# Kernel optimization log

Measured on AMD Instinct MI355X. Metric: run time of the kernel, lower is better.

Reference implementation:

```python
import jax, jax.numpy as jnp
import numpy as np

LEAK_VALUE = 0.1
B, N_ATOMS, IN_F, H, MAX_VAL, OUT_F = 256, 128, 128, 256, 6, 256


def gru(x, W_ih, W_hh, b_ih, b_hh):
    # x: [B, T, in]; W_ih: [3H, in]; W_hh: [3H, H]; gate order r,z,n (torch)
    Bb, T, _ = x.shape
    Hh = W_hh.shape[1]
    x_proj = jnp.einsum('bti,gi->btg', x, W_ih) + b_ih  # [B, T, 3H]

    def step(h, xp):
        gh = h @ W_hh.T + b_hh                      # [B, 3H]
        xr, xz, xn = jnp.split(xp, 3, axis=-1)
        hr, hz, hn = jnp.split(gh, 3, axis=-1)
        r = jax.nn.sigmoid(xr + hr)
        z = jax.nn.sigmoid(xz + hz)
        n = jnp.tanh(xn + r * hn)
        h_new = (1.0 - z) * n + z * h
        return h_new, h_new

    h0 = jnp.zeros((Bb, Hh), x.dtype)
    _, out = jax.lax.scan(step, h0, jnp.swapaxes(x_proj, 0, 1))  # [T, B, H]
    return jnp.swapaxes(out, 0, 1)  # [B, T, H]


def setup_inputs() -> dict:
    key = jax.random.key(0)
    ks = jax.random.split(key, 8)
    s = 0.05
    return {
        'x': jax.random.normal(ks[0], (B, N_ATOMS, IN_F), jnp.float32),
        'bonded_atoms': jax.random.randint(ks[1], (B, N_ATOMS, MAX_VAL), 0, N_ATOMS),
        'W_ih': jax.random.normal(ks[2], (3 * H, IN_F), jnp.float32) * s,
        'W_hh': jax.random.normal(ks[3], (3 * H, H), jnp.float32) * s,
        'b_ih': jax.random.normal(ks[4], (3 * H,), jnp.float32) * s,
        'b_hh': jax.random.normal(ks[5], (3 * H,), jnp.float32) * s,
        'W_fc': jax.random.normal(ks[6], (OUT_F, H * MAX_VAL), jnp.float32) * s,
        'b_fc': jax.random.normal(ks[7], (OUT_F,), jnp.float32) * s,
    }


def reference(x, bonded_atoms, W_ih, W_hh, b_ih, b_hh, W_fc, b_fc):
    rnn_out = gru(x, W_ih, W_hh, b_ih, b_hh)               # [B, N, H]
    batch_idx = jnp.arange(x.shape[0])[:, None, None]       # [B, 1, 1]
    fc_in = rnn_out[batch_idx, bonded_atoms]                # [B, N, V, H] gather
    fc_in = fc_in.reshape(x.shape[0], x.shape[1], -1)       # [B, N, V*H]
    out = fc_in @ W_fc.T + b_fc                             # [B, N, OUT_F]
    return jnp.where(out >= 0, out, LEAK_VALUE * out)
```

## Files before the change

### kernel.cpp

```cpp
#include <hip/hip_runtime.h>
#include <hip/hip_bf16.h>
#include <stdint.h>

typedef unsigned short u16;
typedef __bf16 bf16_t;
typedef bf16_t bf16x8 __attribute__((ext_vector_type(8)));
typedef u16    u16x8  __attribute__((ext_vector_type(8)));
typedef u16    u16x4  __attribute__((ext_vector_type(4)));
typedef float  f32x4  __attribute__((ext_vector_type(4)));

#define BSZ    256
#define NATOMS 128
#define INF    128
#define HH     256
#define H3     768
#define MAXV   6
#define OUTF   256
#define KFC    (HH * MAXV)
#define PLANE  8388608
#define HAP    264

__device__ __forceinline__ u16 f2bf(float f) {
  union { float f; unsigned u; } v; v.f = f;
  unsigned u = v.u;
  unsigned r = (u + 0x7FFFu + ((u >> 16) & 1u)) >> 16;
  return (u16)r;
}
__device__ __forceinline__ float bf2f(u16 h) {
  union { unsigned u; float f; } v; v.u = ((unsigned)h) << 16;
  return v.f;
}
__device__ __forceinline__ f32x4 mfma_bf16(u16x8 a, u16x8 b, f32x4 c) {
  return __builtin_amdgcn_mfma_f32_16x16x32_bf16(
      __builtin_bit_cast(bf16x8, a), __builtin_bit_cast(bf16x8, b), c, 0, 0, 0);
}
__device__ __forceinline__ float sel4(float a0, float a1, float a2, float a3, int q) {
  float t01 = (q & 1) ? a1 : a0;
  float t23 = (q & 1) ? a3 : a2;
  return (q & 2) ? t23 : t01;
}

#define NX4   1048576
#define C1    1048576
#define C2    1073152
#define C3    1122304
#define C4    1220608
__global__ void k_prep4(const float* __restrict__ x, const float* __restrict__ wih,
                        const float* __restrict__ whh, const float* __restrict__ wfc,
                        u16* __restrict__ xb, u16* __restrict__ wihb,
                        u16* __restrict__ whhb, u16* __restrict__ wfcb) {
  int i = blockIdx.x * 256 + threadIdx.x;
  const float* src; u16* dst; int j;
  if (i < C1)      { src = x;   dst = xb;   j = i; }
  else if (i < C2) { src = wih; dst = wihb; j = i - C1; }
  else if (i < C3) { src = whh; dst = whhb; j = i - C2; }
  else             { src = wfc; dst = wfcb; j = i - C3; }
  f32x4 v = *(const f32x4*)(src + (size_t)j * 4);
  u16x4 o;
#pragma unroll
  for (int k = 0; k < 4; k++) o[k] = f2bf(v[k]);
  *(u16x4*)(dst + (size_t)j * 4) = o;
}

__global__ __launch_bounds__(256) void k_xproj(const u16* __restrict__ X,
                                               const u16* __restrict__ W,
                                               const float* __restrict__ bias,
                                               const float* __restrict__ bhh,
                                               u16* __restrict__ out) {
  __shared__ __align__(16) u16 As[128][136];
  __shared__ __align__(16) u16 Bs[128][136];
  const int tid = threadIdx.x, lane = tid & 63, wid = tid >> 6;
  const int c16 = lane & 15, quad = lane >> 4;
  const int wm = (wid & 1) * 64, wn = (wid >> 1) * 64;
  const int bg = blockIdx.x >> 2, tg = blockIdx.x & 3;
  const int n0 = blockIdx.y * 128;

#pragma unroll
  for (int j = 0; j < 8; j++) {
    const int u = tid + j * 256, row = u >> 4, ch = u & 15;
    const int b = bg * 4 + (row & 3), t = tg * 32 + (row >> 2);
    *(u16x8*)&As[row][ch * 8] =
        *(const u16x8*)(X + ((size_t)b * 16384 + t * 128 + ch * 8));
    *(u16x8*)&Bs[row][ch * 8] =
        *(const u16x8*)(W + ((size_t)(n0 + row) * 128 + ch * 8));
  }
  __syncthreads();

  const f32x4 zero = {0.f, 0.f, 0.f, 0.f};
  f32x4 acc[4][4];
#pragma unroll
  for (int mi = 0; mi < 4; mi++)
#pragma unroll
    for (int ni = 0; ni < 4; ni++) acc[mi][ni] = zero;

#pragma unroll
  for (int kt = 0; kt < 4; kt++) {
    u16x8 af[4], bf[4];
#pragma unroll
    for (int mi = 0; mi < 4; mi++)
      af[mi] = *(const u16x8*)&As[wm + mi * 16 + c16][kt * 32 + quad * 8];
#pragma unroll
    for (int ni = 0; ni < 4; ni++)
      bf[ni] = *(const u16x8*)&Bs[wn + ni * 16 + c16][kt * 32 + quad * 8];
#pragma unroll
    for (int mi = 0; mi < 4; mi++)
#pragma unroll
      for (int ni = 0; ni < 4; ni++)
        acc[mi][ni] = mfma_bf16(af[mi], bf[ni], acc[mi][ni]);
  }

  const int bb = bg >> 2, mbh = bg & 3;
#pragma unroll
  for (int ni = 0; ni < 4; ni++) {
    const int n = n0 + wn + ni * 16 + c16;
    const int g = n >> 8, ww = (n >> 5) & 7, pp = (n >> 4) & 1, cc = n & 15;
    const float badd = bias[n] + (g < 2 ? bhh[n] : 0.f);
    u16* plane = out + (size_t)g * PLANE;
#pragma unroll
    for (int mi = 0; mi < 4; mi++) {
      const int t = tg * 32 + (wm >> 2) + mi * 4 + quad;
      u16x4 sv;
#pragma unroll
      for (int r_ = 0; r_ < 4; r_++) sv[r_] = f2bf(acc[mi][ni][r_] + badd);
      *(u16x4*)(plane + (((size_t)((bb * 128 + t) * 8 + ww)) << 9) +
                (mbh * 16 + cc) * 8 + pp * 4) = sv;
    }
  }
}

__global__ void __attribute__((amdgpu_flat_work_group_size(256, 256),
                               amdgpu_waves_per_eu(1, 1)))
k_gru(const u16* __restrict__ Whh, const float* __restrict__ bhh,
      const u16* __restrict__ xp2, u16* __restrict__ rnn) {
  __shared__ __align__(16) u16 hA[2][4 * HAP];
  __shared__ __align__(16) u16 wS[4][12][3][512];
  const int tid = threadIdx.x, lane = tid & 63, w = tid >> 6;
  const int c = lane & 15, q = lane >> 4;
  const int b0 = blockIdx.x * 4;
  const int bb = blockIdx.x >> 2;
  const int Lq = (blockIdx.x & 3) * 16 + c;

  for (int i = tid; i < 2 * 4 * HAP; i += 256) ((u16*)hA)[i] = 0;

  u16x8 wf[12][5];
#pragma unroll
  for (int nt = 0; nt < 12; nt++)
#pragma unroll
    for (int kt = 0; kt < 5; kt++) {
      const int n = (nt >> 2) * 256 + w * 64 + (nt & 3) * 16 + c;
      wf[nt][kt] = *(const u16x8*)(Whh + (size_t)n * HH + kt * 32 + q * 8);
    }
#pragma unroll
  for (int nt = 0; nt < 12; nt++)
#pragma unroll
    for (int kt = 0; kt < 5; kt++) asm volatile("" : "+a"(wf[nt][kt]));

#pragma unroll
  for (int nt = 0; nt < 12; nt++)
#pragma unroll
    for (int kts = 0; kts < 3; kts++) {
      const int n = (nt >> 2) * 256 + w * 64 + (nt & 3) * 16 + c;
      *(u16x8*)&wS[w][nt][kts][lane * 8] =
          *(const u16x8*)(Whh + (size_t)n * HH + (5 + kts) * 32 + q * 8);
    }

  const int col = w * 64 + q * 16 + c;
  const float bhhn = bhh[512 + col];
  float hreg[4] = {0.f, 0.f, 0.f, 0.f};

  const u16* gbase = xp2 + ((size_t)(bb * 128) * 8 + (w * 2 + (q >> 1))) * 512 +
                     (size_t)Lq * 8 + (q & 1) * 4;
  const int sl = lane & 31;
  u16* rnn_base = rnn + ((size_t)(b0 + w) * NATOMS) * HH + sl * 8;

  u16x4 xg0[3], xg1[3];
#pragma unroll
  for (int g = 0; g < 3; g++) xg0[g] = *(const u16x4*)(gbase + (size_t)g * PLANE);
#pragma unroll
  for (int g = 0; g < 3; g++) xg1[g] = *(const u16x4*)(gbase + 4096 + (size_t)g * PLANE);
  const u16* gpre = gbase + 2 * 4096;

  asm volatile("s_waitcnt lgkmcnt(0)\n\ts_barrier" ::: "memory");

  const f32x4 zero4 = {0.f, 0.f, 0.f, 0.f};

  auto step = [&](const int t, u16x4 (&xgc)[3]) {
    const u16* hc = hA[t & 1];
    u16* hnx = hA[(t + 1) & 1];

    if (t && lane < 32) {
      const u16x8 hv8 = *(const u16x8*)&hc[w * HAP + sl * 8];
      *(u16x8*)(rnn_base + (size_t)(t - 1) * HH) = hv8;
    }

    u16x4 xg[3];
#pragma unroll
    for (int g = 0; g < 3; g++) xg[g] = xgc[g];
    if (t < NATOMS - 2) {
#pragma unroll
      for (int g = 0; g < 3; g++)
        xgc[g] = *(const u16x4*)(gpre + (size_t)g * PLANE);
    }

    f32x4 acc[12];
    u16x8 a0 = *(const u16x8*)&hc[(c & 3) * HAP + q * 8];
#pragma unroll
    for (int kt = 0; kt < 8; kt++) {
      u16x8 a1;
      if (kt < 7)
        a1 = *(const u16x8*)&hc[(c & 3) * HAP + (kt + 1) * 32 + q * 8];
      if (kt == 0) {
#pragma unroll
        for (int nt = 0; nt < 12; nt++) acc[nt] = mfma_bf16(a0, wf[nt][0], zero4);
      } else if (kt < 5) {
#pragma unroll
        for (int nt = 0; nt < 12; nt++) acc[nt] = mfma_bf16(a0, wf[nt][kt], acc[nt]);
      } else {
        u16x8 wb[12];
#pragma unroll
        for (int nt = 0; nt < 12; nt++)
          wb[nt] = *(const u16x8*)&wS[w][nt][kt - 5][lane * 8];
#pragma unroll
        for (int nt = 0; nt < 12; nt++) acc[nt] = mfma_bf16(a0, wb[nt], acc[nt]);
      }
      a0 = a1;
    }

#pragma unroll
    for (int r_ = 0; r_ < 4; r_++) {
      const float Ar = sel4(acc[0][r_], acc[1][r_], acc[2][r_], acc[3][r_], q);
      const float Az = sel4(acc[4][r_], acc[5][r_], acc[6][r_], acc[7][r_], q);
      const float An = sel4(acc[8][r_], acc[9][r_], acc[10][r_], acc[11][r_], q);
      const float ar = Ar + bf2f(xg[0][r_]);
      const float az = Az + bf2f(xg[1][r_]);
      const float hn = An + bhhn;
      const float xn = bf2f(xg[2][r_]);
      const float rr = 1.f / (1.f + __expf(-ar));
      const float zz = 1.f / (1.f + __expf(-az));
      const float e  = __expf(2.f * (xn + rr * hn));
      const float nn = 1.f - 2.f / (e + 1.f);
      const float hv = nn + zz * (hreg[r_] - nn);
      hreg[r_] = hv;
      hnx[r_ * HAP + col] = f2bf(hv);
    }

    asm volatile("s_waitcnt lgkmcnt(0)\n\ts_barrier" ::: "memory");
  };

#pragma unroll 1
  for (int tt = 0; tt < NATOMS; tt += 2) {
    step(tt, xg0);
    gpre += 4096;
    step(tt + 1, xg1);
    gpre += 4096;
  }

  if (lane < 32) {
    const u16x8 hv8 = *(const u16x8*)&hA[0][w * HAP + sl * 8];
    *(u16x8*)(rnn_base + (size_t)(NATOMS - 1) * HH) = hv8;
  }
}

__global__ __launch_bounds__(256) void k_fc(const u16* __restrict__ rnn,
                                            const int* __restrict__ bonded,
                                            const u16* __restrict__ W,
                                            const float* __restrict__ bias,
                                            float* __restrict__ out) {
  __shared__ __align__(16) u16 As[2][128][72];
  __shared__ __align__(16) u16 Bs[2][128][72];
  __shared__ int ic[128][6];
  const int tid = threadIdx.x, lane = tid & 63, wid = tid >> 6;
  const int c16 = lane & 15, quad = lane >> 4;
  const int wNm = (wid & 1) * 64;
  const int wNa = (wid >> 1) * 64;
  const int bx = blockIdx.x, n0 = blockIdx.y * 128;
  const int srow = tid >> 3, sch = tid & 7;

  for (int u = tid; u < 768; u += 256) {
    const int v = u >> 7, row = u & 127;
    ic[row][v] = bonded[(size_t)(bx * 128 + row) * MAXV + v];
  }
  __syncthreads();

  u16x8 ra[4], rb[4];
#define STAGE_LOAD(IT)                                                         \
  {                                                                            \
    const int kk_ = (IT) * 64, v_ = kk_ >> 8, kr_ = kk_ & 255;                 \
    _Pragma("unroll")                                                          \
    for (int j = 0; j < 4; j++) {                                              \
      const int row_ = srow + j * 32;                                          \
      const int idx_ = ic[row_][v_];                                           \
      ra[j] = *(const u16x8*)(rnn + ((size_t)(bx * 128 + idx_)) * HH + kr_ +   \
                              sch * 8);                                        \
      rb[j] = *(const u16x8*)(W + (size_t)(n0 + row_) * KFC + kk_ + sch * 8);  \
    }                                                                          \
  }
#define STAGE_WRITE(B_)                                                        \
  {                                                                            \
    _Pragma("unroll")                                                          \
    for (int j = 0; j < 4; j++) {                                              \
      const int row_ = srow + j * 32;                                          \
      *(u16x8*)&As[B_][row_][sch * 8] = ra[j];                                 \
      *(u16x8*)&Bs[B_][row_][sch * 8] = rb[j];                                 \
    }                                                                          \
  }

  STAGE_LOAD(0);
  STAGE_WRITE(0);
  __syncthreads();

  const f32x4 zero = {0.f, 0.f, 0.f, 0.f};
  f32x4 acc[4][4];
#pragma unroll
  for (int mi = 0; mi < 4; mi++)
#pragma unroll
    for (int ni = 0; ni < 4; ni++) acc[mi][ni] = zero;

#pragma unroll 1
  for (int it = 0; it < 24; it++) {
    const int cur = it & 1;
    if (it < 23) STAGE_LOAD(it + 1);
#pragma unroll
    for (int kt = 0; kt < 2; kt++) {
      u16x8 aw[4], ba[4];
#pragma unroll
      for (int mi = 0; mi < 4; mi++)
        aw[mi] = *(const u16x8*)&Bs[cur][wNm + mi * 16 + c16][kt * 32 + quad * 8];
#pragma unroll
      for (int ni = 0; ni < 4; ni++)
        ba[ni] = *(const u16x8*)&As[cur][wNa + ni * 16 + c16][kt * 32 + quad * 8];
#pragma unroll
      for (int mi = 0; mi < 4; mi++)
#pragma unroll
        for (int ni = 0; ni < 4; ni++)
          acc[mi][ni] = mfma_bf16(aw[mi], ba[ni], acc[mi][ni]);
    }
    if (it < 23) STAGE_WRITE(cur ^ 1);
    __syncthreads();
  }

#pragma unroll
  for (int mi = 0; mi < 4; mi++) {
    const int n = n0 + wNm + mi * 16 + quad * 4;
    const f32x4 bv = *(const f32x4*)(bias + n);
#pragma unroll
    for (int ni = 0; ni < 4; ni++) {
      const int mm = bx * 128 + wNa + ni * 16 + c16;
      f32x4 vv;
#pragma unroll
      for (int r_ = 0; r_ < 4; r_++) {
        const float t = acc[mi][ni][r_] + bv[r_];
        vv[r_] = t >= 0.f ? t : 0.1f * t;
      }
      *(f32x4*)(out + (size_t)mm * OUTF + n) = vv;
    }
  }
}

extern "C" void kernel_launch(void* const* d_in, const int* in_sizes, int n_in,
                              void* d_out, int out_size, void* d_ws, size_t ws_size,
                              hipStream_t stream) {
  const float* x      = (const float*)d_in[0];
  const int*   bonded = (const int*)d_in[1];
  const float* Wih    = (const float*)d_in[2];
  const float* Whh    = (const float*)d_in[3];
  const float* bih    = (const float*)d_in[4];
  const float* bhh    = (const float*)d_in[5];
  const float* Wfc    = (const float*)d_in[6];
  const float* bfc    = (const float*)d_in[7];
  float* out = (float*)d_out;

  char* ws = (char*)d_ws;
  u16* xp2  = (u16*)(ws);
  u16* rnn  = (u16*)(ws + 50331648);
  u16* whhb = (u16*)(ws + 67108864);
  u16* wfcb = (u16*)(ws + 67502080);
  u16* xb   = (u16*)(ws + 68288512);
  u16* wihb = (u16*)(ws + 76677120);

  k_prep4<<<C4 / 256, 256, 0, stream>>>(x, Wih, Whh, Wfc, xb, wihb, whhb, wfcb);
  k_xproj<<<dim3(256, 6), 256, 0, stream>>>(xb, wihb, bih, bhh, xp2);
  k_gru<<<64, 256, 0, stream>>>(whhb, bhh, xp2, rnn);
  k_fc<<<dim3(256, 2), 256, 0, stream>>>(rnn, bonded, wfcb, bfc, out);
}
```

Before: 351.6 us.

## Keep full W_hh slice resident in AGPRs and pre-swizzle weights in prep

```diff
diff --git a/kernel.cpp b/kernel.cpp
--- a/kernel.cpp
+++ b/kernel.cpp
@@ -59,7 +59,16 @@
   u16x4 o;
 #pragma unroll
   for (int k = 0; k < 4; k++) o[k] = f2bf(v[k]);
-  *(u16x4*)(dst + (size_t)j * 4) = o;
+  if (i >= C2 && i < C3) {
+    const int E = j * 4, n = E >> 8, k = E & 255;
+    const int g = n >> 8, nr = n & 255;
+    const int w = nr >> 6, nt = g * 4 + ((nr >> 4) & 3), c = nr & 15;
+    const int kt = k >> 5, q = (k >> 3) & 3, e = k & 7;
+    *(u16x4*)(whhb + (size_t)((((w * 12 + nt) * 8 + kt) << 9) +
+                              (q * 16 + c) * 8 + e)) = o;
+  } else {
+    *(u16x4*)(dst + (size_t)j * 4) = o;
+  }
 }
 
 __global__ __launch_bounds__(256) void k_xproj(const u16* __restrict__ X,
@@ -133,36 +142,25 @@
 k_gru(const u16* __restrict__ Whh, const float* __restrict__ bhh,
       const u16* __restrict__ xp2, u16* __restrict__ rnn) {
   __shared__ __align__(16) u16 hA[2][4 * HAP];
-  __shared__ __align__(16) u16 wS[4][12][3][512];
   const int tid = threadIdx.x, lane = tid & 63, w = tid >> 6;
   const int c = lane & 15, q = lane >> 4;
   const int b0 = blockIdx.x * 4;
   const int bb = blockIdx.x >> 2;
   const int Lq = (blockIdx.x & 3) * 16 + c;
 
-  for (int i = tid; i < 2 * 4 * HAP; i += 256) ((u16*)hA)[i] = 0;
-
-  u16x8 wf[12][5];
+  for (int i = tid; i < 4 * HAP; i += 256) hA[0][i] = 0;
+
+  u16x8 wf[12][8];
 #pragma unroll
   for (int nt = 0; nt < 12; nt++)
 #pragma unroll
-    for (int kt = 0; kt < 5; kt++) {
-      const int n = (nt >> 2) * 256 + w * 64 + (nt & 3) * 16 + c;
-      wf[nt][kt] = *(const u16x8*)(Whh + (size_t)n * HH + kt * 32 + q * 8);
-    }
+    for (int kt = 0; kt < 8; kt++)
+      wf[nt][kt] = *(const u16x8*)(Whh + (size_t)((((w * 12 + nt) * 8 + kt) << 9) +
+                                                  lane * 8));
 #pragma unroll
   for (int nt = 0; nt < 12; nt++)
 #pragma unroll
-    for (int kt = 0; kt < 5; kt++) asm volatile("" : "+a"(wf[nt][kt]));
-
-#pragma unroll
-  for (int nt = 0; nt < 12; nt++)
-#pragma unroll
-    for (int kts = 0; kts < 3; kts++) {
-      const int n = (nt >> 2) * 256 + w * 64 + (nt & 3) * 16 + c;
-      *(u16x8*)&wS[w][nt][kts][lane * 8] =
-          *(const u16x8*)(Whh + (size_t)n * HH + (5 + kts) * 32 + q * 8);
-    }
+    for (int kt = 0; kt < 8; kt++) asm volatile("" : "+a"(wf[nt][kt]));
 
   const int col = w * 64 + q * 16 + c;
   const float bhhn = bhh[512 + col];
@@ -187,11 +185,6 @@
   auto step = [&](const int t, u16x4 (&xgc)[3]) {
     const u16* hc = hA[t & 1];
     u16* hnx = hA[(t + 1) & 1];
-
-    if (t && lane < 32) {
-      const u16x8 hv8 = *(const u16x8*)&hc[w * HAP + sl * 8];
-      *(u16x8*)(rnn_base + (size_t)(t - 1) * HH) = hv8;
-    }
 
     u16x4 xg[3];
 #pragma unroll
@@ -212,18 +205,16 @@
       if (kt == 0) {
 #pragma unroll
         for (int nt = 0; nt < 12; nt++) acc[nt] = mfma_bf16(a0, wf[nt][0], zero4);
-      } else if (kt < 5) {
+      } else {
 #pragma unroll
         for (int nt = 0; nt < 12; nt++) acc[nt] = mfma_bf16(a0, wf[nt][kt], acc[nt]);
-      } else {
-        u16x8 wb[12];
-#pragma unroll
-        for (int nt = 0; nt < 12; nt++)
-          wb[nt] = *(const u16x8*)&wS[w][nt][kt - 5][lane * 8];
-#pragma unroll
-        for (int nt = 0; nt < 12; nt++) acc[nt] = mfma_bf16(a0, wb[nt], acc[nt]);
       }
       a0 = a1;
+    }
+
+    if (t && lane < 32) {
+      const u16x8 hv8 = *(const u16x8*)&hc[w * HAP + sl * 8];
+      *(u16x8*)(rnn_base + (size_t)(t - 1) * HH) = hv8;
     }
 
 #pragma unroll
```

New measurement: 430.5 us. 22.4% more time.
